# Kernel optimization log

Hardware: AMD Instinct MI355X
Metric: run time of the kernel (lower is better)

Reference implementation:

```python
import jax, jax.numpy as jnp
import numpy as np

B, S, D, H = 2, 2048, 2048, 16
DH = D // H


def setup_inputs() -> dict:
    key = jax.random.key(0)
    k1, k2, k3 = jax.random.split(key, 3)
    x = jax.random.normal(k1, (B, S, D), dtype=jnp.float32)
    Wqkv = jax.random.normal(k2, (D, 3 * D), dtype=jnp.float32) * (1.0 / np.sqrt(D))
    bqkv = jnp.zeros((3 * D,), dtype=jnp.float32)
    Wproj = jax.random.normal(k3, (D, D), dtype=jnp.float32) * (1.0 / np.sqrt(D))
    bproj = jnp.zeros((D,), dtype=jnp.float32)
    return {"x": x, "Wqkv": Wqkv, "bqkv": bqkv, "Wproj": Wproj, "bproj": bproj}


def reference(x, Wqkv, bqkv, Wproj, bproj):
    b, s, d = x.shape
    h, dh = H, DH
    # fused qkv projection: [b, s, 3, h, dh]
    qkv = (x @ Wqkv + bqkv).reshape(b, s, 3, h, dh)
    q, k, v = qkv[:, :, 0], qkv[:, :, 1], qkv[:, :, 2]  # each [b, s, h, dh]
    scale = 1.0 / np.sqrt(dh).astype(np.float32)
    # scores [b, h, q, k]
    attn = jnp.einsum('bqhd,bkhd->bhqk', q, k) * scale
    causal = jnp.tril(jnp.ones((s, s), dtype=bool))  # [s, s]
    attn = jnp.where(causal[None, None], attn, -jnp.inf)
    attn = jax.nn.softmax(attn, axis=-1)
    out = jnp.einsum('bhqk,bkhd->bqhd', attn, v).reshape(b, s, d)
    return out @ Wproj + bproj
```

## Files before the change

### kernel.cpp

```cpp
#include <hip/hip_runtime.h>
#include <hip/hip_bf16.h>

#define BB 2
#define SS 2048
#define DD 2048
#define HH 16
#define DHH 128
#define MM 4096
#define NN1 6144
#define NTILES (DD / 64)

typedef __attribute__((ext_vector_type(8))) short bf16x8;
typedef __attribute__((ext_vector_type(4))) float f32x4;
typedef unsigned int u32;

static __device__ __forceinline__ float exp2_hw(float x) {
  return __builtin_amdgcn_exp2f(x);
}

static __device__ __forceinline__ unsigned short f2bf(float f) {
  union { float f; u32 u; } v; v.f = f;
  return (unsigned short)((v.u + 0x7FFFu + ((v.u >> 16) & 1u)) >> 16);
}

static __device__ __forceinline__ void gload_lds16(const void* g, void* l) {
  __builtin_amdgcn_global_load_lds((const __attribute__((address_space(1))) u32*)g,
                                   (__attribute__((address_space(3))) u32*)l, 16, 0, 0);
}

__global__ __launch_bounds__(256) void k_cvt(const float* __restrict__ in,
                                             unsigned short* __restrict__ out) {
  int i = blockIdx.x * 256 + threadIdx.x;
  float4 v = ((const float4*)in)[i];
  ushort4 o;
  o.x = f2bf(v.x); o.y = f2bf(v.y); o.z = f2bf(v.z); o.w = f2bf(v.w);
  ((ushort4*)out)[i] = o;
}

__global__ __launch_bounds__(256) void k_transpose(const float* __restrict__ in,
                                                   unsigned short* __restrict__ out,
                                                   int R, int C) {
  __shared__ float t[32][33];
  int bx = blockIdx.x * 32, by = blockIdx.y * 32;
  int tx = threadIdx.x, ty = threadIdx.y;
  #pragma unroll
  for (int i = ty; i < 32; i += 8)
    t[i][tx] = in[(size_t)(by + i) * C + bx + tx];
  __syncthreads();
  #pragma unroll
  for (int i = ty; i < 32; i += 8)
    out[(size_t)(bx + i) * R + by + tx] = f2bf(t[tx][i]);
}

__device__ __forceinline__ void gemm_core(const char* __restrict__ Ag,
                                          const char* __restrict__ Bg,
                                          char* Alds, char* Blds,
                                          f32x4 acc[4][4]) {
  const int tid = threadIdx.x;
  const int wave = tid >> 6, lane = tid & 63;
  const int g = lane >> 4, c = lane & 15;
  const int wm = wave >> 1, wn = wave & 1;

  auto stageA = [&](int buf, int kt) {
    #pragma unroll
    for (int q = 0; q < 4; ++q) {
      int off = q * 8192 + wave * 1024 + (lane << 4);
      int row = off >> 7, cb = off & 127;
      gload_lds16(Ag + (size_t)row * 4096 + kt * 128 + (cb ^ ((row & 7) << 4)),
                  Alds + buf * 32768 + q * 8192 + wave * 1024);
    }
  };
  auto stageB = [&](int buf, int kt) {
    #pragma unroll
    for (int q = 0; q < 2; ++q) {
      int off = q * 8192 + wave * 1024 + (lane << 4);
      int row = off >> 7, cb = off & 127;
      gload_lds16(Bg + (size_t)row * 4096 + kt * 128 + (cb ^ ((row & 7) << 4)),
                  Blds + buf * 16384 + q * 8192 + wave * 1024);
    }
  };

  stageA(0, 0); stageB(0, 0);
  stageA(1, 1); stageB(1, 1);
  asm volatile("s_waitcnt vmcnt(6)" ::: "memory");
  __builtin_amdgcn_sched_barrier(0);
  __builtin_amdgcn_s_barrier();

  for (int t = 0; t < NTILES; ++t) {
    const int buf = t % 3;
    const char* Ab = Alds + buf * 32768;
    const char* Bb = Blds + buf * 16384;
    bf16x8 af[4][2], b0[2][2];
    #pragma unroll
    for (int i = 0; i < 4; ++i) {
      int row = wm * 64 + i * 16 + c;
      #pragma unroll
      for (int kk = 0; kk < 2; ++kk)
        af[i][kk] = *(const bf16x8*)(Ab + row * 128 + ((kk * 64 + g * 16) ^ ((row & 7) << 4)));
    }
    #pragma unroll
    for (int j = 0; j < 2; ++j) {
      int row = wn * 64 + j * 16 + c;
      #pragma unroll
      for (int kk = 0; kk < 2; ++kk)
        b0[j][kk] = *(const bf16x8*)(Bb + row * 128 + ((kk * 64 + g * 16) ^ ((row & 7) << 4)));
    }
    if (t + 2 < NTILES) stageA((t + 2) % 3, t + 2);
    __builtin_amdgcn_s_barrier();
    asm volatile("s_waitcnt lgkmcnt(0)" ::: "memory");
    __builtin_amdgcn_sched_barrier(0);
    __builtin_amdgcn_s_setprio(1);
    #pragma unroll
    for (int i = 0; i < 4; ++i)
      #pragma unroll
      for (int j = 0; j < 2; ++j)
        #pragma unroll
        for (int kk = 0; kk < 2; ++kk)
          acc[i][j] = __builtin_amdgcn_mfma_f32_16x16x32_bf16(af[i][kk], b0[j][kk], acc[i][j], 0, 0, 0);
    __builtin_amdgcn_s_setprio(0);
    __builtin_amdgcn_s_barrier();
    bf16x8 b1[2][2];
    #pragma unroll
    for (int j = 0; j < 2; ++j) {
      int row = wn * 64 + (2 + j) * 16 + c;
      #pragma unroll
      for (int kk = 0; kk < 2; ++kk)
        b1[j][kk] = *(const bf16x8*)(Bb + row * 128 + ((kk * 64 + g * 16) ^ ((row & 7) << 4)));
    }
    if (t + 2 < NTILES) stageB((t + 2) % 3, t + 2);
    __builtin_amdgcn_s_barrier();
    asm volatile("s_waitcnt lgkmcnt(0)" ::: "memory");
    __builtin_amdgcn_sched_barrier(0);
    __builtin_amdgcn_s_setprio(1);
    #pragma unroll
    for (int i = 0; i < 4; ++i)
      #pragma unroll
      for (int j = 0; j < 2; ++j)
        #pragma unroll
        for (int kk = 0; kk < 2; ++kk)
          acc[i][j + 2] = __builtin_amdgcn_mfma_f32_16x16x32_bf16(af[i][kk], b1[j][kk], acc[i][j + 2], 0, 0, 0);
    __builtin_amdgcn_s_setprio(0);
    if (t < NTILES - 1) {
      if (t + 2 < NTILES) { asm volatile("s_waitcnt vmcnt(6)" ::: "memory"); }
      else                { asm volatile("s_waitcnt vmcnt(0)" ::: "memory"); }
      __builtin_amdgcn_sched_barrier(0);
      __builtin_amdgcn_s_barrier();
    }
  }
}

__global__ __launch_bounds__(512, 1) void k_gemm1(const unsigned short* __restrict__ A,
                                                  const unsigned short* __restrict__ Bt,
                                                  const float* __restrict__ bias,
                                                  unsigned short* __restrict__ Qb,
                                                  unsigned short* __restrict__ Kb,
                                                  unsigned short* __restrict__ Vt) {
  __shared__ __align__(16) char lds[147456];
  const int n0 = blockIdx.x * 128, m0 = blockIdx.y * 256;
  f32x4 acc[4][4] = {};
  gemm_core((const char*)A + (size_t)m0 * 4096,
            (const char*)Bt + (size_t)n0 * 4096,
            lds, lds + 98304, acc);
  const int lane = threadIdx.x & 63, wave = threadIdx.x >> 6;
  const int g = lane >> 4, c = lane & 15;
  const int wm = wave >> 1, wn = wave & 1;
  const int head = (n0 >> 7) & 15, which = n0 >> 11;
  const float qsc = 0.12751879523263566f;
  #pragma unroll
  for (int i = 0; i < 4; ++i) {
    int rowb = m0 + wm * 64 + i * 16 + g * 4;
    int bb = rowb >> 11, s = rowb & 2047;
    #pragma unroll
    for (int j = 0; j < 4; ++j) {
      int dh = wn * 64 + j * 16 + c;
      float bv = bias[n0 + dh];
      if (which == 2) {
        ushort4 p;
        p.x = f2bf(acc[i][j][0] + bv);
        p.y = f2bf(acc[i][j][1] + bv);
        p.z = f2bf(acc[i][j][2] + bv);
        p.w = f2bf(acc[i][j][3] + bv);
        *(ushort4*)(Vt + ((size_t)(bb * HH + head) * DHH + dh) * SS + s) = p;
      } else {
        float v0 = acc[i][j][0] + bv, v1 = acc[i][j][1] + bv;
        float v2 = acc[i][j][2] + bv, v3 = acc[i][j][3] + bv;
        if (which == 0) { v0 *= qsc; v1 *= qsc; v2 *= qsc; v3 *= qsc; }
        unsigned short* dst = (which == 0 ? Qb : Kb) + ((size_t)(bb * HH + head) * SS + s) * DHH + dh;
        dst[0]       = f2bf(v0);
        dst[DHH]     = f2bf(v1);
        dst[2 * DHH] = f2bf(v2);
        dst[3 * DHH] = f2bf(v3);
      }
    }
  }
}

__global__ __launch_bounds__(512, 1) void k_gemm2(const unsigned short* __restrict__ A,
                                                  const unsigned short* __restrict__ Bt,
                                                  const float* __restrict__ bias,
                                                  float* __restrict__ out) {
  __shared__ __align__(16) char lds[147456];
  const int n0 = blockIdx.x * 128, m0 = blockIdx.y * 256;
  f32x4 acc[4][4] = {};
  gemm_core((const char*)A + (size_t)m0 * 4096,
            (const char*)Bt + (size_t)n0 * 4096,
            lds, lds + 98304, acc);
  const int lane = threadIdx.x & 63, wave = threadIdx.x >> 6;
  const int g = lane >> 4, c = lane & 15;
  const int wm = wave >> 1, wn = wave & 1;
  #pragma unroll
  for (int i = 0; i < 4; ++i) {
    int rowb = m0 + wm * 64 + i * 16 + g * 4;
    #pragma unroll
    for (int j = 0; j < 4; ++j) {
      int gcol = n0 + wn * 64 + j * 16 + c;
      float bv = bias[gcol];
      #pragma unroll
      for (int r = 0; r < 4; ++r)
        out[(size_t)(rowb + r) * DD + gcol] = acc[i][j][r] + bv;
    }
  }
}

__global__ __launch_bounds__(256, 2) void k_attn(const unsigned short* __restrict__ Qb,
                                                 const unsigned short* __restrict__ Kb,
                                                 const unsigned short* __restrict__ Vt,
                                                 unsigned short* __restrict__ O) {
  __shared__ __align__(16) unsigned short Kt[2][64 * 128];
  __shared__ __align__(16) unsigned short Vs[2][128 * 64];
  __shared__ __align__(16) unsigned short Pl[4][32 * 64];
  const int qtl = (blockIdx.y < 16) ? blockIdx.x : (15 - blockIdx.x);
  const int bh = blockIdx.y;
  const int b = bh >> 4, h = bh & 15;
  const int tid = threadIdx.x, wave = tid >> 6, lane = tid & 63;
  const int g = lane >> 4, c = lane & 15;
  const int q0w = qtl * 128 + wave * 32;
  const unsigned short* Qp = Qb + (size_t)bh * SS * DHH;
  const unsigned short* Kp = Kb + (size_t)bh * SS * DHH;
  const unsigned short* Vp = Vt + (size_t)bh * DHH * SS;

  bf16x8 qf[2][4];
  #pragma unroll
  for (int m = 0; m < 2; ++m)
    #pragma unroll
    for (int ks = 0; ks < 4; ++ks)
      qf[m][ks] = *(const bf16x8*)(Qp + (size_t)(q0w + m * 16 + c) * DHH + ks * 32 + g * 8);

  f32x4 acc[2][8] = {};
  float mrow[2] = {-1e30f, -1e30f}, lsum[2] = {0.f, 0.f};

  auto stage = [&](int buf, int kv0) {
    #pragma unroll
    for (int r = 0; r < 4; ++r) {
      int base = r * 4096 + wave * 1024;
      int off = base + (lane << 4);
      { int row = off >> 8; int cb = (off & 255) ^ ((row & 7) << 4);
        gload_lds16((const char*)Kp + (size_t)(kv0 + row) * 256 + cb,
                    (char*)Kt[buf] + base); }
      { int row = off >> 7; int cb = (off & 127) ^ ((row & 7) << 4);
        gload_lds16((const char*)Vp + (size_t)row * (SS * 2) + (size_t)kv0 * 2 + cb,
                    (char*)Vs[buf] + base); }
    }
  };

  const int ntiles = 2 * qtl + 2;
  stage(0, 0);
  __syncthreads();

  for (int t = 0; t < ntiles; ++t) {
    const int cur = t & 1;
    const int kv0 = t * 64;
    if (t + 1 < ntiles) stage(cur ^ 1, kv0 + 64);
    if (kv0 <= q0w + 31) {
      const unsigned short* K_ = Kt[cur];
      const unsigned short* V_ = Vs[cur];
      f32x4 sa[2][4] = {};
      __builtin_amdgcn_s_setprio(1);
      #pragma unroll
      for (int nb = 0; nb < 4; ++nb) {
        const int rk = nb * 16 + c;
        const int swz = (rk & 7) << 4;
        #pragma unroll
        for (int ks = 0; ks < 4; ++ks) {
          bf16x8 kf = *(const bf16x8*)((const char*)K_ + rk * 256 + ((ks * 64 + g * 16) ^ swz));
          sa[0][nb] = __builtin_amdgcn_mfma_f32_16x16x32_bf16(kf, qf[0][ks], sa[0][nb], 0, 0, 0);
          sa[1][nb] = __builtin_amdgcn_mfma_f32_16x16x32_bf16(kf, qf[1][ks], sa[1][nb], 0, 0, 0);
        }
      }
      __builtin_amdgcn_s_setprio(0);
      #pragma unroll
      for (int m = 0; m < 2; ++m) {
        const int q = q0w + m * 16 + c;
        float p[4][4];
        float tm = -1e30f;
        #pragma unroll
        for (int nb = 0; nb < 4; ++nb)
          #pragma unroll
          for (int r = 0; r < 4; ++r) {
            float s = sa[m][nb][r];
            if (kv0 + nb * 16 + g * 4 + r > q) s = -1e30f;
            p[nb][r] = s;
            tm = fmaxf(tm, s);
          }
        tm = fmaxf(tm, __shfl_xor(tm, 16, 64));
        tm = fmaxf(tm, __shfl_xor(tm, 32, 64));
        float mr = mrow[m];
        if (__any(tm > mr + 11.0f)) {
          float mnew = fmaxf(mr, tm);
          float sf = exp2_hw(mr - mnew);
          lsum[m] *= sf;
          float sfr[4];
          #pragma unroll
          for (int r = 0; r < 4; ++r)
            sfr[r] = __shfl(sf, 20 * g + r, 64);
          #pragma unroll
          for (int nf = 0; nf < 8; ++nf)
            #pragma unroll
            for (int r = 0; r < 4; ++r) acc[m][nf][r] *= sfr[r];
          mrow[m] = mnew; mr = mnew;
        }
        float rs = 0.f;
        #pragma unroll
        for (int nb = 0; nb < 4; ++nb)
          #pragma unroll
          for (int r = 0; r < 4; ++r) {
            p[nb][r] = exp2_hw(p[nb][r] - mr);
            rs += p[nb][r];
          }
        rs += __shfl_xor(rs, 16, 64);
        rs += __shfl_xor(rs, 32, 64);
        lsum[m] += rs;
        const int rowp = m * 16 + c;
        const int swzp = (rowp & 7) << 4;
        #pragma unroll
        for (int nb = 0; nb < 4; ++nb)
          #pragma unroll
          for (int i2 = 0; i2 < 2; ++i2) {
            u32 w = (u32)f2bf(p[nb][2 * i2]) | ((u32)f2bf(p[nb][2 * i2 + 1]) << 16);
            *(u32*)((char*)Pl[wave] + rowp * 128 + (((nb * 16 + g * 4 + 2 * i2) * 2) ^ swzp)) = w;
          }
      }
      asm volatile("s_waitcnt lgkmcnt(0)" ::: "memory");
      __builtin_amdgcn_sched_barrier(0);
      bf16x8 pf[2][2];
      #pragma unroll
      for (int m = 0; m < 2; ++m)
        #pragma unroll
        for (int c2 = 0; c2 < 2; ++c2) {
          int rowp = m * 16 + c;
          pf[m][c2] = *(const bf16x8*)((const char*)Pl[wave] + rowp * 128 +
                                       ((c2 * 64 + g * 16) ^ ((rowp & 7) << 4)));
        }
      __builtin_amdgcn_s_setprio(1);
      #pragma unroll
      for (int nf = 0; nf < 8; ++nf) {
        const int rv = nf * 16 + c;
        const int swzv = (rv & 7) << 4;
        #pragma unroll
        for (int c2 = 0; c2 < 2; ++c2) {
          bf16x8 vf = *(const bf16x8*)((const char*)V_ + rv * 128 + ((c2 * 64 + g * 16) ^ swzv));
          acc[0][nf] = __builtin_amdgcn_mfma_f32_16x16x32_bf16(pf[0][c2], vf, acc[0][nf], 0, 0, 0);
          acc[1][nf] = __builtin_amdgcn_mfma_f32_16x16x32_bf16(pf[1][c2], vf, acc[1][nf], 0, 0, 0);
        }
      }
      __builtin_amdgcn_s_setprio(0);
    }
    __syncthreads();
  }

  unsigned short* Op = O + (size_t)b * SS * DD + (size_t)h * DHH;
  #pragma unroll
  for (int m = 0; m < 2; ++m) {
    float inv = 1.0f / lsum[m];
    float invr[4];
    #pragma unroll
    for (int r = 0; r < 4; ++r)
      invr[r] = __shfl(inv, 20 * g + r, 64);
    #pragma unroll
    for (int nf = 0; nf < 8; ++nf)
      #pragma unroll
      for (int r = 0; r < 4; ++r) {
        int q = q0w + m * 16 + g * 4 + r;
        Op[(size_t)q * DD + nf * 16 + c] = f2bf(acc[m][nf][r] * invr[r]);
      }
  }
}

extern "C" void kernel_launch(void* const* d_in, const int* in_sizes, int n_in,
                              void* d_out, int out_size, void* d_ws, size_t ws_size,
                              hipStream_t stream) {
  const float* x     = (const float*)d_in[0];
  const float* Wqkv  = (const float*)d_in[1];
  const float* bqkv  = (const float*)d_in[2];
  const float* Wproj = (const float*)d_in[3];
  const float* bproj = (const float*)d_in[4];
  float* out = (float*)d_out;

  char* ws = (char*)d_ws;
  unsigned short* xb  = (unsigned short*)ws; ws += (size_t)MM * DD * 2;
  unsigned short* w1t = (unsigned short*)ws; ws += (size_t)NN1 * DD * 2;
  unsigned short* w2t = (unsigned short*)ws; ws += (size_t)DD * DD * 2;
  unsigned short* Qb  = (unsigned short*)ws; ws += (size_t)BB * HH * SS * DHH * 2;
  unsigned short* Kb  = (unsigned short*)ws; ws += (size_t)BB * HH * SS * DHH * 2;
  unsigned short* Vt  = (unsigned short*)ws; ws += (size_t)BB * HH * SS * DHH * 2;
  unsigned short* Ob  = (unsigned short*)ws; ws += (size_t)MM * DD * 2;

  k_cvt<<<dim3((MM * DD) / 1024), 256, 0, stream>>>(x, xb);
  k_transpose<<<dim3(NN1 / 32, DD / 32), dim3(32, 8), 0, stream>>>(Wqkv, w1t, DD, NN1);
  k_transpose<<<dim3(DD / 32, DD / 32), dim3(32, 8), 0, stream>>>(Wproj, w2t, DD, DD);
  k_gemm1<<<dim3(NN1 / 128, MM / 256), 512, 0, stream>>>(xb, w1t, bqkv, Qb, Kb, Vt);
  k_attn<<<dim3(SS / 128, BB * HH), 256, 0, stream>>>(Qb, Kb, Vt, Ob);
  k_gemm2<<<dim3(DD / 128, MM / 256), 512, 0, stream>>>(Ob, w2t, bproj, out);
}
```

Baseline: 268.8 us.

## Shrink GEMM tiles to 128x128 with 4 waves, K=32 stages, and XCD-aware block swizzle

Both projection GEMMs move from a 256x128 tile with 8 waves and 64-wide K stages to a 128x128 tile with 4 waves and 32-wide K stages. The LDS footprint drops from 144KB to 48KB, so launch bounds allow three blocks per CU. Block IDs are remapped so consecutive blocks spread across the 8 XCDs while keeping neighbouring tiles together for L2 reuse. The aim is better occupancy and latency hiding, at the cost of lower arithmetic intensity per tile and more barriers per unit of K work.

Result: slower. 293.0 us (+9.0%).

```diff
diff --git a/kernel.cpp b/kernel.cpp
--- a/kernel.cpp
+++ b/kernel.cpp
@@ -8,7 +8,7 @@
 #define DHH 128
 #define MM 4096
 #define NN1 6144
-#define NTILES (DD / 64)
+#define KT32 64
 
 typedef __attribute__((ext_vector_type(8))) short bf16x8;
 typedef __attribute__((ext_vector_type(4))) float f32x4;
@@ -52,10 +52,10 @@
     out[(size_t)(bx + i) * R + by + tx] = f2bf(t[tx][i]);
 }
 
-__device__ __forceinline__ void gemm_core(const char* __restrict__ Ag,
-                                          const char* __restrict__ Bg,
-                                          char* Alds, char* Blds,
-                                          f32x4 acc[4][4]) {
+__device__ __forceinline__ void gemm_core128(const char* __restrict__ Ag,
+                                             const char* __restrict__ Bg,
+                                             char* Alds, char* Blds,
+                                             f32x4 acc[4][4]) {
   const int tid = threadIdx.x;
   const int wave = tid >> 6, lane = tid & 63;
   const int g = lane >> 4, c = lane & 15;
@@ -63,104 +63,82 @@
 
   auto stageA = [&](int buf, int kt) {
     #pragma unroll
-    for (int q = 0; q < 4; ++q) {
-      int off = q * 8192 + wave * 1024 + (lane << 4);
-      int row = off >> 7, cb = off & 127;
-      gload_lds16(Ag + (size_t)row * 4096 + kt * 128 + (cb ^ ((row & 7) << 4)),
-                  Alds + buf * 32768 + q * 8192 + wave * 1024);
+    for (int q = 0; q < 2; ++q) {
+      int off = q * 4096 + tid * 16;
+      int row = off >> 6, cb = off & 63;
+      gload_lds16(Ag + (size_t)row * 4096 + kt * 64 + (cb ^ (((row >> 1) & 3) << 4)),
+                  Alds + buf * 8192 + q * 4096 + wave * 1024);
     }
   };
   auto stageB = [&](int buf, int kt) {
     #pragma unroll
     for (int q = 0; q < 2; ++q) {
-      int off = q * 8192 + wave * 1024 + (lane << 4);
-      int row = off >> 7, cb = off & 127;
-      gload_lds16(Bg + (size_t)row * 4096 + kt * 128 + (cb ^ ((row & 7) << 4)),
-                  Blds + buf * 16384 + q * 8192 + wave * 1024);
+      int off = q * 4096 + tid * 16;
+      int row = off >> 6, cb = off & 63;
+      gload_lds16(Bg + (size_t)row * 4096 + kt * 64 + (cb ^ (((row >> 1) & 3) << 4)),
+                  Blds + buf * 8192 + q * 4096 + wave * 1024);
     }
   };
 
   stageA(0, 0); stageB(0, 0);
   stageA(1, 1); stageB(1, 1);
-  asm volatile("s_waitcnt vmcnt(6)" ::: "memory");
+  asm volatile("s_waitcnt vmcnt(4)" ::: "memory");
   __builtin_amdgcn_sched_barrier(0);
   __builtin_amdgcn_s_barrier();
 
-  for (int t = 0; t < NTILES; ++t) {
-    const int buf = t % 3;
-    const char* Ab = Alds + buf * 32768;
-    const char* Bb = Blds + buf * 16384;
-    bf16x8 af[4][2], b0[2][2];
+  int buf = 0;
+  for (int t = 0; t < KT32; ++t) {
+    const char* Ab = Alds + buf * 8192;
+    const char* Bb = Blds + buf * 8192;
+    bf16x8 af[4], bf[4];
     #pragma unroll
     for (int i = 0; i < 4; ++i) {
       int row = wm * 64 + i * 16 + c;
-      #pragma unroll
-      for (int kk = 0; kk < 2; ++kk)
-        af[i][kk] = *(const bf16x8*)(Ab + row * 128 + ((kk * 64 + g * 16) ^ ((row & 7) << 4)));
-    }
-    #pragma unroll
-    for (int j = 0; j < 2; ++j) {
+      af[i] = *(const bf16x8*)(Ab + row * 64 + ((g * 16) ^ (((row >> 1) & 3) << 4)));
+    }
+    #pragma unroll
+    for (int j = 0; j < 4; ++j) {
       int row = wn * 64 + j * 16 + c;
-      #pragma unroll
-      for (int kk = 0; kk < 2; ++kk)
-        b0[j][kk] = *(const bf16x8*)(Bb + row * 128 + ((kk * 64 + g * 16) ^ ((row & 7) << 4)));
-    }
-    if (t + 2 < NTILES) stageA((t + 2) % 3, t + 2);
-    __builtin_amdgcn_s_barrier();
+      bf[j] = *(const bf16x8*)(Bb + row * 64 + ((g * 16) ^ (((row >> 1) & 3) << 4)));
+    }
+    if (t + 2 < KT32) {
+      int nb = buf + 2; if (nb >= 3) nb -= 3;
+      stageA(nb, t + 2);
+      stageB(nb, t + 2);
+    }
     asm volatile("s_waitcnt lgkmcnt(0)" ::: "memory");
     __builtin_amdgcn_sched_barrier(0);
     __builtin_amdgcn_s_setprio(1);
     #pragma unroll
     for (int i = 0; i < 4; ++i)
       #pragma unroll
-      for (int j = 0; j < 2; ++j)
-        #pragma unroll
-        for (int kk = 0; kk < 2; ++kk)
-          acc[i][j] = __builtin_amdgcn_mfma_f32_16x16x32_bf16(af[i][kk], b0[j][kk], acc[i][j], 0, 0, 0);
+      for (int j = 0; j < 4; ++j)
+        acc[i][j] = __builtin_amdgcn_mfma_f32_16x16x32_bf16(af[i], bf[j], acc[i][j], 0, 0, 0);
     __builtin_amdgcn_s_setprio(0);
-    __builtin_amdgcn_s_barrier();
-    bf16x8 b1[2][2];
-    #pragma unroll
-    for (int j = 0; j < 2; ++j) {
-      int row = wn * 64 + (2 + j) * 16 + c;
-      #pragma unroll
-      for (int kk = 0; kk < 2; ++kk)
-        b1[j][kk] = *(const bf16x8*)(Bb + row * 128 + ((kk * 64 + g * 16) ^ ((row & 7) << 4)));
-    }
-    if (t + 2 < NTILES) stageB((t + 2) % 3, t + 2);
-    __builtin_amdgcn_s_barrier();
-    asm volatile("s_waitcnt lgkmcnt(0)" ::: "memory");
-    __builtin_amdgcn_sched_barrier(0);
-    __builtin_amdgcn_s_setprio(1);
-    #pragma unroll
-    for (int i = 0; i < 4; ++i)
-      #pragma unroll
-      for (int j = 0; j < 2; ++j)
-        #pragma unroll
-        for (int kk = 0; kk < 2; ++kk)
-          acc[i][j + 2] = __builtin_amdgcn_mfma_f32_16x16x32_bf16(af[i][kk], b1[j][kk], acc[i][j + 2], 0, 0, 0);
-    __builtin_amdgcn_s_setprio(0);
-    if (t < NTILES - 1) {
-      if (t + 2 < NTILES) { asm volatile("s_waitcnt vmcnt(6)" ::: "memory"); }
-      else                { asm volatile("s_waitcnt vmcnt(0)" ::: "memory"); }
+    if (t < KT32 - 1) {
+      if (t < KT32 - 2) { asm volatile("s_waitcnt vmcnt(4)" ::: "memory"); }
+      else              { asm volatile("s_waitcnt vmcnt(0)" ::: "memory"); }
       __builtin_amdgcn_sched_barrier(0);
       __builtin_amdgcn_s_barrier();
     }
-  }
-}
-
-__global__ __launch_bounds__(512, 1) void k_gemm1(const unsigned short* __restrict__ A,
+    ++buf; if (buf == 3) buf = 0;
+  }
+}
+
+__global__ __launch_bounds__(256, 3) void k_gemm1(const unsigned short* __restrict__ A,
                                                   const unsigned short* __restrict__ Bt,
                                                   const float* __restrict__ bias,
                                                   unsigned short* __restrict__ Qb,
                                                   unsigned short* __restrict__ Kb,
                                                   unsigned short* __restrict__ Vt) {
-  __shared__ __align__(16) char lds[147456];
-  const int n0 = blockIdx.x * 128, m0 = blockIdx.y * 256;
+  __shared__ __align__(16) char lds[49152];
+  const int bid = blockIdx.x;
+  const int sid = (bid & 7) * 192 + (bid >> 3);
+  const int n0 = (sid % 48) * 128, m0 = (sid / 48) * 128;
   f32x4 acc[4][4] = {};
-  gemm_core((const char*)A + (size_t)m0 * 4096,
-            (const char*)Bt + (size_t)n0 * 4096,
-            lds, lds + 98304, acc);
+  gemm_core128((const char*)A + (size_t)m0 * 4096,
+               (const char*)Bt + (size_t)n0 * 4096,
+               lds, lds + 24576, acc);
   const int lane = threadIdx.x & 63, wave = threadIdx.x >> 6;
   const int g = lane >> 4, c = lane & 15;
   const int wm = wave >> 1, wn = wave & 1;
@@ -195,16 +173,18 @@
   }
 }
 
-__global__ __launch_bounds__(512, 1) void k_gemm2(const unsigned short* __restrict__ A,
+__global__ __launch_bounds__(256, 3) void k_gemm2(const unsigned short* __restrict__ A,
                                                   const unsigned short* __restrict__ Bt,
                                                   const float* __restrict__ bias,
                                                   float* __restrict__ out) {
-  __shared__ __align__(16) char lds[147456];
-  const int n0 = blockIdx.x * 128, m0 = blockIdx.y * 256;
+  __shared__ __align__(16) char lds[49152];
+  const int bid = blockIdx.x;
+  const int sid = (bid & 7) * 64 + (bid >> 3);
+  const int n0 = (sid % 16) * 128, m0 = (sid / 16) * 128;
   f32x4 acc[4][4] = {};
-  gemm_core((const char*)A + (size_t)m0 * 4096,
-            (const char*)Bt + (size_t)n0 * 4096,
-            lds, lds + 98304, acc);
+  gemm_core128((const char*)A + (size_t)m0 * 4096,
+               (const char*)Bt + (size_t)n0 * 4096,
+               lds, lds + 24576, acc);
   const int lane = threadIdx.x & 63, wave = threadIdx.x >> 6;
   const int g = lane >> 4, c = lane & 15;
   const int wm = wave >> 1, wn = wave & 1;
@@ -408,7 +388,7 @@
   k_cvt<<<dim3((MM * DD) / 1024), 256, 0, stream>>>(x, xb);
   k_transpose<<<dim3(NN1 / 32, DD / 32), dim3(32, 8), 0, stream>>>(Wqkv, w1t, DD, NN1);
   k_transpose<<<dim3(DD / 32, DD / 32), dim3(32, 8), 0, stream>>>(Wproj, w2t, DD, DD);
-  k_gemm1<<<dim3(NN1 / 128, MM / 256), 512, 0, stream>>>(xb, w1t, bqkv, Qb, Kb, Vt);
+  k_gemm1<<<dim3(1536), 256, 0, stream>>>(xb, w1t, bqkv, Qb, Kb, Vt);
   k_attn<<<dim3(SS / 128, BB * HH), 256, 0, stream>>>(Qb, Kb, Vt, Ob);
-  k_gemm2<<<dim3(DD / 128, MM / 256), 512, 0, stream>>>(Ob, w2t, bproj, out);
-}
+  k_gemm2<<<dim3(512), 256, 0, stream>>>(Ob, w2t, bproj, out);
+}
```

## Split GEMM k-loop into k-halves and overlap LDS reads with MFMA

Applied to the files above, without the earlier changes.

Restructures the per-tile GEMM inner loop so it is split along the k dimension instead of the N dimension. All A and B fragments for the first k-half are loaded, then the second half is issued, and the first 16 MFMAs start after a partial lgkmcnt wait. Both global-to-LDS stages are issued together, and the two intra-tile s_barriers are dropped. The aim is to overlap LDS reads with MFMA work and cut synchronisation. In exchange it holds more fragment registers live and relies on the hand-counted waitcnt being correct.

Result: no change. 265.4 us (-1.3%).

```diff
diff --git a/kernel.cpp b/kernel.cpp
--- a/kernel.cpp
+++ b/kernel.cpp
@@ -90,55 +90,50 @@
     const int buf = t % 3;
     const char* Ab = Alds + buf * 32768;
     const char* Bb = Blds + buf * 16384;
-    bf16x8 af[4][2], b0[2][2];
+    bf16x8 af[4][2], bfv[4][2];
     #pragma unroll
     for (int i = 0; i < 4; ++i) {
       int row = wm * 64 + i * 16 + c;
-      #pragma unroll
-      for (int kk = 0; kk < 2; ++kk)
-        af[i][kk] = *(const bf16x8*)(Ab + row * 128 + ((kk * 64 + g * 16) ^ ((row & 7) << 4)));
-    }
-    #pragma unroll
-    for (int j = 0; j < 2; ++j) {
+      af[i][0] = *(const bf16x8*)(Ab + row * 128 + ((g * 16) ^ ((row & 7) << 4)));
+    }
+    #pragma unroll
+    for (int j = 0; j < 4; ++j) {
       int row = wn * 64 + j * 16 + c;
-      #pragma unroll
-      for (int kk = 0; kk < 2; ++kk)
-        b0[j][kk] = *(const bf16x8*)(Bb + row * 128 + ((kk * 64 + g * 16) ^ ((row & 7) << 4)));
-    }
-    if (t + 2 < NTILES) stageA((t + 2) % 3, t + 2);
-    __builtin_amdgcn_s_barrier();
+      bfv[j][0] = *(const bf16x8*)(Bb + row * 128 + ((g * 16) ^ ((row & 7) << 4)));
+    }
+    __builtin_amdgcn_sched_barrier(0);
+    #pragma unroll
+    for (int i = 0; i < 4; ++i) {
+      int row = wm * 64 + i * 16 + c;
+      af[i][1] = *(const bf16x8*)(Ab + row * 128 + ((64 + g * 16) ^ ((row & 7) << 4)));
+    }
+    #pragma unroll
+    for (int j = 0; j < 4; ++j) {
+      int row = wn * 64 + j * 16 + c;
+      bfv[j][1] = *(const bf16x8*)(Bb + row * 128 + ((64 + g * 16) ^ ((row & 7) << 4)));
+    }
+    if (t + 2 < NTILES) {
+      int nb = buf + 2; if (nb >= 3) nb -= 3;
+      stageA(nb, t + 2);
+      stageB(nb, t + 2);
+    }
+    asm volatile("s_waitcnt lgkmcnt(8)" ::: "memory");
+    __builtin_amdgcn_sched_barrier(0);
+    __builtin_amdgcn_s_setprio(1);
+    #pragma unroll
+    for (int i = 0; i < 4; ++i)
+      #pragma unroll
+      for (int j = 0; j < 4; ++j)
+        acc[i][j] = __builtin_amdgcn_mfma_f32_16x16x32_bf16(af[i][0], bfv[j][0], acc[i][j], 0, 0, 0);
+    __builtin_amdgcn_s_setprio(0);
     asm volatile("s_waitcnt lgkmcnt(0)" ::: "memory");
     __builtin_amdgcn_sched_barrier(0);
     __builtin_amdgcn_s_setprio(1);
     #pragma unroll
     for (int i = 0; i < 4; ++i)
       #pragma unroll
-      for (int j = 0; j < 2; ++j)
-        #pragma unroll
-        for (int kk = 0; kk < 2; ++kk)
-          acc[i][j] = __builtin_amdgcn_mfma_f32_16x16x32_bf16(af[i][kk], b0[j][kk], acc[i][j], 0, 0, 0);
-    __builtin_amdgcn_s_setprio(0);
-    __builtin_amdgcn_s_barrier();
-    bf16x8 b1[2][2];
-    #pragma unroll
-    for (int j = 0; j < 2; ++j) {
-      int row = wn * 64 + (2 + j) * 16 + c;
-      #pragma unroll
-      for (int kk = 0; kk < 2; ++kk)
-        b1[j][kk] = *(const bf16x8*)(Bb + row * 128 + ((kk * 64 + g * 16) ^ ((row & 7) << 4)));
-    }
-    if (t + 2 < NTILES) stageB((t + 2) % 3, t + 2);
-    __builtin_amdgcn_s_barrier();
-    asm volatile("s_waitcnt lgkmcnt(0)" ::: "memory");
-    __builtin_amdgcn_sched_barrier(0);
-    __builtin_amdgcn_s_setprio(1);
-    #pragma unroll
-    for (int i = 0; i < 4; ++i)
-      #pragma unroll
-      for (int j = 0; j < 2; ++j)
-        #pragma unroll
-        for (int kk = 0; kk < 2; ++kk)
-          acc[i][j + 2] = __builtin_amdgcn_mfma_f32_16x16x32_bf16(af[i][kk], b1[j][kk], acc[i][j + 2], 0, 0, 0);
+      for (int j = 0; j < 4; ++j)
+        acc[i][j] = __builtin_amdgcn_mfma_f32_16x16x32_bf16(af[i][1], bfv[j][1], acc[i][j], 0, 0, 0);
     __builtin_amdgcn_s_setprio(0);
     if (t < NTILES - 1) {
       if (t + 2 < NTILES) { asm volatile("s_waitcnt vmcnt(6)" ::: "memory"); }
```
